# Kernel tuning notes

Measured on AMD Instinct MI355X. Metric: run time of the kernel, lower is better.

Reference implementation:

```python
import jax, jax.numpy as jnp
import numpy as np
from jax import lax

B, C_IN, C_OUT, K, N_W, L = 32, 256, 256, 7, 8, 4096
SQ = C_IN // 32  # squeezed dim = 8
STRIDE, PAD = 1, 3


def setup_inputs() -> dict:
    key = jax.random.key(0)
    ks = jax.random.split(key, 8)
    s = 0.05
    return {
        "x": jax.random.normal(ks[0], (B, C_IN, L), dtype=jnp.float32),
        "conv_weight": jax.random.normal(ks[1], (C_OUT, C_IN, K, N_W), dtype=jnp.float32) * s,
        "w1": jax.random.normal(ks[2], (C_IN, SQ), dtype=jnp.float32) * s,   # linear1 weight (x @ w1)
        "b1": jax.random.normal(ks[3], (SQ,), dtype=jnp.float32) * s,
        "wk": jax.random.normal(ks[4], (SQ, K), dtype=jnp.float32) * s,      # kernel head
        "wi": jax.random.normal(ks[5], (SQ, C_IN), dtype=jnp.float32) * s,   # inc head
        "wo": jax.random.normal(ks[6], (SQ, C_OUT), dtype=jnp.float32) * s,  # outc head
        "wn": jax.random.normal(ks[7], (SQ, N_W), dtype=jnp.float32) * s,    # nums head
    }


def reference(x, conv_weight, w1, b1, wk, wi, wo, wn):
    # SqueezeFeedForward: AdaptiveAvgPool1d(1) == mean over length, then Linear + exact GELU
    pooled = jnp.mean(x, axis=-1)                        # [B, C_in]
    h = jax.nn.gelu(pooled @ w1 + b1, approximate=False)  # [B, SQ]

    kr = jax.nn.sigmoid(h @ wk)          # [B, K]
    inc = jax.nn.sigmoid(h @ wi)         # [B, C_in]
    outc = jax.nn.sigmoid(h @ wo)        # [B, C_out]
    nums = jax.nn.softmax(h @ wn, -1)    # [B, N_w]

    # Per-sample mixed weights: sum over num_weight of 4-way outer-product gated base weight
    w = jnp.einsum('bk,bi,bo,bn,oikn->boik', kr, inc, outc, nums, conv_weight)  # [B,O,I,K]

    b, o, i, k = w.shape
    l = x.shape[-1]
    # Batched per-sample conv via grouped conv: groups = B
    lhs = x.reshape(1, b * i, l)         # [1, B*I, L]
    rhs = w.reshape(b * o, i, k)         # [B*O, I, K]
    out = lax.conv_general_dilated(
        lhs, rhs,
        window_strides=(STRIDE,),
        padding=[(PAD, PAD)],
        dimension_numbers=('NCH', 'OIH', 'NCH'),
        feature_group_count=b,
    )
    return out.reshape(b, o, -1)         # [B, O, L_out]
```

## Files before the change

### kernel.cpp

```cpp
#include <hip/hip_runtime.h>
#include <hip/hip_bf16.h>
#include <math.h>

#define B_   32
#define CI   256
#define CO   256
#define KW   7
#define NW   8
#define SQD  8
#define L_   4096
#define PITCH 272

typedef __attribute__((ext_vector_type(8))) __bf16 bf16x8;
typedef __attribute__((ext_vector_type(4))) __bf16 bf16x4;
typedef __attribute__((ext_vector_type(4))) float  f32x4;

static __device__ __forceinline__ unsigned short f2bf(float f) {
    unsigned int u = __builtin_bit_cast(unsigned int, f);
    u += 0x7FFFu + ((u >> 16) & 1u);
    return (unsigned short)(u >> 16);
}
static __device__ __forceinline__ uint2 pack4bf(float a, float b, float c, float d) {
    bf16x4 v;
    v[0] = (__bf16)a; v[1] = (__bf16)b; v[2] = (__bf16)c; v[3] = (__bf16)d;
    return __builtin_bit_cast(uint2, v);
}

__global__ __launch_bounds__(256) void k1_mean(
        const float* __restrict__ x, float* __restrict__ pooled) {
    int row = blockIdx.x;
    const float* p = x + (size_t)row * L_;
    int t = threadIdx.x;
    float s = 0.f;
#pragma unroll
    for (int it = 0; it < 4; ++it) {
        float4 v = *(const float4*)(p + (size_t)(t + 256 * it) * 4);
        s += v.x + v.y + v.z + v.w;
    }
    for (int m = 1; m <= 32; m <<= 1) s += __shfl_xor(s, m);
    __shared__ float wsum[4];
    if ((t & 63) == 0) wsum[t >> 6] = s;
    __syncthreads();
    if (t == 0)
        pooled[row] = (wsum[0] + wsum[1] + wsum[2] + wsum[3]) * (1.0f / L_);
}

__global__ __launch_bounds__(64) void k2_gates(
        const float* __restrict__ pooled,
        const float* __restrict__ w1, const float* __restrict__ b1,
        const float* __restrict__ wk, const float* __restrict__ wi,
        const float* __restrict__ wo, const float* __restrict__ wn,
        float* __restrict__ kr, float* __restrict__ inc,
        float* __restrict__ outc, float* __restrict__ nums)
{
    int b = blockIdx.x, lane = threadIdx.x;
    float pc[4];
#pragma unroll
    for (int j = 0; j < 4; ++j)
        pc[j] = pooled[b * CI + lane + 64 * j];
    float h[SQD];
#pragma unroll
    for (int s = 0; s < SQD; ++s) {
        float ps = 0.f;
#pragma unroll
        for (int j = 0; j < 4; ++j)
            ps += pc[j] * w1[(lane + 64 * j) * SQD + s];
        for (int m = 1; m <= 32; m <<= 1) ps += __shfl_xor(ps, m);
        float z = ps + b1[s];
        h[s] = 0.5f * z * (1.0f + erff(z * 0.70710678118654752f));
    }
    if (lane < KW) {
        float a = 0.f;
#pragma unroll
        for (int s = 0; s < SQD; ++s) a += h[s] * wk[s * KW + lane];
        kr[b * 8 + lane] = 1.0f / (1.0f + expf(-a));
    }
    if (lane < NW) {
        float e[NW]; float mx = -1e30f;
#pragma unroll
        for (int n = 0; n < NW; ++n) {
            float a = 0.f;
#pragma unroll
            for (int s = 0; s < SQD; ++s) a += h[s] * wn[s * NW + n];
            e[n] = a; mx = fmaxf(mx, a);
        }
        float den = 0.f;
#pragma unroll
        for (int n = 0; n < NW; ++n) den += expf(e[n] - mx);
        nums[b * NW + lane] = expf(e[lane] - mx) / den;
    }
#pragma unroll
    for (int j = 0; j < 4; ++j) {
        int c = lane + 64 * j;
        float a = 0.f, o2 = 0.f;
#pragma unroll
        for (int s = 0; s < SQD; ++s) {
            a  += h[s] * wi[s * CI + c];
            o2 += h[s] * wo[s * CO + c];
        }
        inc[b * CI + c]  = 1.0f / (1.0f + expf(-a));
        outc[b * CO + c] = 1.0f / (1.0f + expf(-o2));
    }
}

__global__ __launch_bounds__(256) void k3_wgen(
        const float* __restrict__ cw,
        const float* __restrict__ kr, const float* __restrict__ inc,
        const float* __restrict__ outc, const float* __restrict__ nums,
        unsigned short* __restrict__ W2) {
    __shared__ float s_nums[B_][NW];
    __shared__ float s_kr[B_][KW];
    __shared__ float s_inc[B_][32];
    __shared__ float s_outc[B_][8];
    int t = threadIdx.x;
    int ic = blockIdx.x & 7, o0 = (blockIdx.x >> 3) * 8;
    s_nums[t >> 3][t & 7] = nums[t];
    if (t < B_ * KW) s_kr[t / KW][t % KW] = kr[(t / KW) * 8 + (t % KW)];
    for (int u = t; u < 32 * 32; u += 256) {
        int bb = u >> 5, ii = u & 31;
        s_inc[bb][ii] = inc[bb * CI + ic * 32 + ii];
    }
    for (int u = t; u < 32 * 8; u += 256) {
        int bb = u >> 3, oo = u & 7;
        s_outc[bb][oo] = outc[bb * CO + o0 + oo];
    }
    __syncthreads();
    int ii = t & 31, oo = t >> 5;
    int o = o0 + oo, i = ic * 32 + ii;
    float cwv[KW][NW];
    const float* p = cw + ((size_t)(o * CI + i)) * (KW * NW);
#pragma unroll
    for (int k = 0; k < KW; ++k)
#pragma unroll
        for (int n = 0; n < NW; ++n) cwv[k][n] = p[k * NW + n];
    for (int bb = 0; bb < B_; ++bb) {
        float gio = s_inc[bb][ii] * s_outc[bb][oo];
#pragma unroll
        for (int k = 0; k < KW; ++k) {
            float sk = 0.f;
#pragma unroll
            for (int n = 0; n < NW; ++n) sk += s_nums[bb][n] * cwv[k][n];
            float w = s_kr[bb][k] * gio * sk;
            W2[(((size_t)(bb * KW + k) * 8 + ic) * CO + o) * 32 + ii] = f2bf(w);
        }
    }
}

__global__ __launch_bounds__(256, 2) void k4_conv(
        const float* __restrict__ x,
        const unsigned short* __restrict__ W2,
        float* __restrict__ out) {
    __shared__ __align__(16) unsigned short xs[134 * PITCH];
    int bid = blockIdx.x;
    int wg  = (bid & 7) * 128 + (bid >> 3);
    int b = wg >> 5, l0 = (wg & 31) * 128;
    int t = threadIdx.x;
    const float* xb = x + (size_t)b * CI * L_;

    {
        int u = t >> 3;
        int lam = t & 7;
        int i0 = u * 8;
#pragma unroll
        for (int it = 0; it < 4; ++it) {
            int ch = lam + 8 * it;
            const float* src = xb + (size_t)i0 * L_ + l0 + ch * 4;
            float4 f[8];
#pragma unroll
            for (int e = 0; e < 8; ++e)
                f[e] = *(const float4*)(src + (size_t)e * L_);
#pragma unroll
            for (int j = 0; j < 4; ++j) {
                int r = ch * 4 + j + 3;
                uint2 a = pack4bf((&f[0].x)[j], (&f[1].x)[j], (&f[2].x)[j], (&f[3].x)[j]);
                uint2 c = pack4bf((&f[4].x)[j], (&f[5].x)[j], (&f[6].x)[j], (&f[7].x)[j]);
                uint4 w; w.x = a.x; w.y = a.y; w.z = c.x; w.w = c.y;
                *(uint4*)(xs + r * PITCH + u * 8) = w;
            }
        }
    }
    if (t < 192) {
        int h = t >> 5, u = t & 31;
        int r = (h < 3) ? h : (128 + h);
        int gl = l0 - 3 + r;
        bool ok = (gl >= 0 && gl < L_);
        float f[8];
#pragma unroll
        for (int e = 0; e < 8; ++e)
            f[e] = ok ? xb[(size_t)(u * 8 + e) * L_ + gl] : 0.f;
        uint2 a = pack4bf(f[0], f[1], f[2], f[3]);
        uint2 c = pack4bf(f[4], f[5], f[6], f[7]);
        uint4 w; w.x = a.x; w.y = a.y; w.z = c.x; w.w = c.y;
        *(uint4*)(xs + r * PITCH + u * 8) = w;
    }
    __syncthreads();

    int lane = t & 63, wid = t >> 6;
    int o_half = (wid & 1) * 128;
    int l_half = (wid >> 1) * 64;
    int ml = lane & 15, kg = lane >> 4;

    f32x4 acc[8][4];
#pragma unroll
    for (int a = 0; a < 8; ++a)
#pragma unroll
        for (int c = 0; c < 4; ++c) acc[a][c] = (f32x4){0.f, 0.f, 0.f, 0.f};

    const unsigned short* wA = W2 + (size_t)b * (56 * CO * 32)
                               + (o_half + ml) * 32 + kg * 8;
    const unsigned short* xB = xs + (size_t)(l_half + ml) * PITCH + kg * 8;

    auto LOADF = [&](bf16x8 (&AF)[8], bf16x8 (&BF)[4], int S) {
        int k_ = S >> 3, icc_ = S & 7;
#pragma unroll
        for (int mt = 0; mt < 8; ++mt)
            AF[mt] = *(const bf16x8*)(wA + (size_t)S * (CO * 32) + mt * 16 * 32);
#pragma unroll
        for (int nt = 0; nt < 4; ++nt)
            BF[nt] = *(const bf16x8*)(xB + (nt * 16 + k_) * PITCH + icc_ * 32);
    };
    auto DOMFMA = [&](bf16x8 (&AF)[8], bf16x8 (&BF)[4]) {
        __builtin_amdgcn_s_setprio(1);
#pragma unroll
        for (int mt = 0; mt < 8; ++mt)
#pragma unroll
            for (int nt = 0; nt < 4; ++nt)
                acc[mt][nt] = __builtin_amdgcn_mfma_f32_16x16x32_bf16(
                    AF[mt], BF[nt], acc[mt][nt], 0, 0, 0);
        __builtin_amdgcn_s_setprio(0);
    };

    bf16x8 afA[8], bfA[4], afB[8], bfB[4];
    LOADF(afA, bfA, 0);
    for (int s = 0; s < 56; s += 2) {
        LOADF(afB, bfB, s + 1);
        DOMFMA(afA, bfA);
        if (s + 2 < 56) LOADF(afA, bfA, s + 2);
        DOMFMA(afB, bfB);
    }

#pragma unroll
    for (int mt = 0; mt < 8; ++mt) {
        int o = o_half + mt * 16 + kg * 4;
#pragma unroll
        for (int nt = 0; nt < 4; ++nt) {
            int l = l0 + l_half + nt * 16 + ml;
            float* po = out + ((size_t)(b * CO + o)) * L_ + l;
#pragma unroll
            for (int q = 0; q < 4; ++q)
                po[(size_t)q * L_] = acc[mt][nt][q];
        }
    }
}

extern "C" void kernel_launch(void* const* d_in, const int* in_sizes, int n_in,
                              void* d_out, int out_size, void* d_ws, size_t ws_size,
                              hipStream_t stream) {
    const float* x  = (const float*)d_in[0];
    const float* cw = (const float*)d_in[1];
    const float* w1 = (const float*)d_in[2];
    const float* b1 = (const float*)d_in[3];
    const float* wk = (const float*)d_in[4];
    const float* wi = (const float*)d_in[5];
    const float* wo = (const float*)d_in[6];
    const float* wn = (const float*)d_in[7];
    float* out = (float*)d_out;

    char* ws = (char*)d_ws;
    unsigned short* W2 = (unsigned short*)(ws + 0);
    float* pooled = (float*)(ws + 29360128);
    float* kr     = (float*)(ws + 29392896);
    float* inc    = (float*)(ws + 29393920);
    float* outc   = (float*)(ws + 29426688);
    float* nums   = (float*)(ws + 29459456);

    k1_mean<<<B_ * CI, 256, 0, stream>>>(x, pooled);
    k2_gates<<<B_, 64, 0, stream>>>(pooled, w1, b1, wk, wi, wo, wn,
                                    kr, inc, outc, nums);
    k3_wgen<<<256, 256, 0, stream>>>(cw, kr, inc, outc, nums, W2);
    k4_conv<<<1024, 256, 0, stream>>>(x, W2, out);
}
```

Baseline: 189.4 us.

## Switch conv GEMM to 32x32x16 MFMA with per-wave 64-channel output tiles

Replaces the 16x16x32 bf16 MFMA tiling, where each wave owned a 128x64 output block, with 32x32x16 MFMA and each wave owning 64 output channels across all 128 positions. The K loop is split into 112 half-steps, and each wave starts at a different offset (wid*28) so waves read different weight and LDS regions at the same time. The aim is fewer fragment loads per MFMA, better operand reuse and less LDS bank contention. In exchange the output stores follow the 32x32 accumulator layout, which may coalesce less well, and the wrap-around indexing adds a little scalar work.

```diff
diff --git a/kernel.cpp b/kernel.cpp
--- a/kernel.cpp
+++ b/kernel.cpp
@@ -11,9 +11,10 @@
 #define L_   4096
 #define PITCH 272
 
-typedef __attribute__((ext_vector_type(8))) __bf16 bf16x8;
-typedef __attribute__((ext_vector_type(4))) __bf16 bf16x4;
-typedef __attribute__((ext_vector_type(4))) float  f32x4;
+typedef __attribute__((ext_vector_type(8)))  __bf16 bf16x8;
+typedef __attribute__((ext_vector_type(4)))  __bf16 bf16x4;
+typedef __attribute__((ext_vector_type(4)))  float  f32x4;
+typedef __attribute__((ext_vector_type(16))) float  f32x16;
 
 static __device__ __forceinline__ unsigned short f2bf(float f) {
     unsigned int u = __builtin_bit_cast(unsigned int, f);
@@ -196,61 +197,68 @@
     __syncthreads();
 
     int lane = t & 63, wid = t >> 6;
-    int o_half = (wid & 1) * 128;
-    int l_half = (wid >> 1) * 64;
-    int ml = lane & 15, kg = lane >> 4;
-
-    f32x4 acc[8][4];
-#pragma unroll
-    for (int a = 0; a < 8; ++a)
-#pragma unroll
-        for (int c = 0; c < 4; ++c) acc[a][c] = (f32x4){0.f, 0.f, 0.f, 0.f};
+    int o_base = wid * 64;
+    int ml = lane & 31, khalf = lane >> 5;
+
+    f32x16 acc[2][4];
+#pragma unroll
+    for (int a = 0; a < 2; ++a)
+#pragma unroll
+        for (int c = 0; c < 4; ++c)
+#pragma unroll
+            for (int q = 0; q < 16; ++q) acc[a][c][q] = 0.f;
 
     const unsigned short* wA = W2 + (size_t)b * (56 * CO * 32)
-                               + (o_half + ml) * 32 + kg * 8;
-    const unsigned short* xB = xs + (size_t)(l_half + ml) * PITCH + kg * 8;
-
-    auto LOADF = [&](bf16x8 (&AF)[8], bf16x8 (&BF)[4], int S) {
-        int k_ = S >> 3, icc_ = S & 7;
-#pragma unroll
-        for (int mt = 0; mt < 8; ++mt)
-            AF[mt] = *(const bf16x8*)(wA + (size_t)S * (CO * 32) + mt * 16 * 32);
+                               + (o_base + ml) * 32 + khalf * 8;
+    const unsigned short* xB = xs + (size_t)ml * PITCH + khalf * 8;
+
+    auto LOADF = [&](bf16x8 (&AF)[2], bf16x8 (&BF)[4], int S) {
+        int k_ = S >> 4, icc_ = (S >> 1) & 7, half_ = S & 1;
+        size_t aoff = (size_t)(k_ * 8 + icc_) * (CO * 32) + half_ * 16;
+#pragma unroll
+        for (int mt = 0; mt < 2; ++mt)
+            AF[mt] = *(const bf16x8*)(wA + aoff + mt * 32 * 32);
+        int boff = k_ * PITCH + icc_ * 32 + half_ * 16;
 #pragma unroll
         for (int nt = 0; nt < 4; ++nt)
-            BF[nt] = *(const bf16x8*)(xB + (nt * 16 + k_) * PITCH + icc_ * 32);
+            BF[nt] = *(const bf16x8*)(xB + boff + nt * 32 * PITCH);
     };
-    auto DOMFMA = [&](bf16x8 (&AF)[8], bf16x8 (&BF)[4]) {
+    auto DOMFMA = [&](bf16x8 (&AF)[2], bf16x8 (&BF)[4]) {
         __builtin_amdgcn_s_setprio(1);
 #pragma unroll
-        for (int mt = 0; mt < 8; ++mt)
+        for (int mt = 0; mt < 2; ++mt)
 #pragma unroll
             for (int nt = 0; nt < 4; ++nt)
-                acc[mt][nt] = __builtin_amdgcn_mfma_f32_16x16x32_bf16(
+                acc[mt][nt] = __builtin_amdgcn_mfma_f32_32x32x16_bf16(
                     AF[mt], BF[nt], acc[mt][nt], 0, 0, 0);
         __builtin_amdgcn_s_setprio(0);
     };
 
-    bf16x8 afA[8], bfA[4], afB[8], bfB[4];
-    LOADF(afA, bfA, 0);
-    for (int s = 0; s < 56; s += 2) {
-        LOADF(afB, bfB, s + 1);
+    int base = wid * 28;
+    bf16x8 afA[2], bfA[4], afB[2], bfB[4];
+    LOADF(afA, bfA, base);
+    for (int ss = 0; ss < 112; ss += 2) {
+        int S1 = ss + 1 + base; if (S1 >= 112) S1 -= 112;
+        LOADF(afB, bfB, S1);
         DOMFMA(afA, bfA);
-        if (s + 2 < 56) LOADF(afA, bfA, s + 2);
+        if (ss + 2 < 112) {
+            int S2 = ss + 2 + base; if (S2 >= 112) S2 -= 112;
+            LOADF(afA, bfA, S2);
+        }
         DOMFMA(afB, bfB);
     }
 
 #pragma unroll
-    for (int mt = 0; mt < 8; ++mt) {
-        int o = o_half + mt * 16 + kg * 4;
+    for (int mt = 0; mt < 2; ++mt)
 #pragma unroll
         for (int nt = 0; nt < 4; ++nt) {
-            int l = l0 + l_half + nt * 16 + ml;
-            float* po = out + ((size_t)(b * CO + o)) * L_ + l;
-#pragma unroll
-            for (int q = 0; q < 4; ++q)
-                po[(size_t)q * L_] = acc[mt][nt][q];
-        }
-    }
+            int l = l0 + nt * 32 + ml;
+#pragma unroll
+            for (int q = 0; q < 16; ++q) {
+                int o = o_base + mt * 32 + (q & 3) + 8 * (q >> 2) + 4 * khalf;
+                out[((size_t)(b * CO + o)) * L_ + l] = acc[mt][nt][q];
+            }
+        }
 }
 
 extern "C" void kernel_launch(void* const* d_in, const int* in_sizes, int n_in,
```

After: 194.5 us. 1.03x slower.

## Switch conv GEMM to 32x32x16 MFMA with per-wave full-O tiles

Applied to the files above, without the earlier changes.

Replaces the 16x16x32 bf16 MFMA tiling, where each wave covered a 128(O)x64(L) quadrant, with 32x32x16 MFMAs where each wave covers all 256 output channels for a 32-wide L strip. This reduces B-fragment LDS reads per MFMA and changes the weight-fragment and output-store addressing to match the 32x32 accumulator layout. The LDS pitch also changes from 272 to 264, which may alter bank conflicts. Every wave now reads the full weight slab from global/L2, doubling weight traffic per wave, and the K-loop has twice as many steps.

```diff
diff --git a/kernel.cpp b/kernel.cpp
--- a/kernel.cpp
+++ b/kernel.cpp
@@ -9,11 +9,11 @@
 #define NW   8
 #define SQD  8
 #define L_   4096
-#define PITCH 272
-
-typedef __attribute__((ext_vector_type(8))) __bf16 bf16x8;
-typedef __attribute__((ext_vector_type(4))) __bf16 bf16x4;
-typedef __attribute__((ext_vector_type(4))) float  f32x4;
+#define PITCH 264
+
+typedef __attribute__((ext_vector_type(8)))  __bf16 bf16x8;
+typedef __attribute__((ext_vector_type(4)))  __bf16 bf16x4;
+typedef __attribute__((ext_vector_type(16))) float  f32x16;
 
 static __device__ __forceinline__ unsigned short f2bf(float f) {
     unsigned int u = __builtin_bit_cast(unsigned int, f);
@@ -196,59 +196,54 @@
     __syncthreads();
 
     int lane = t & 63, wid = t >> 6;
-    int o_half = (wid & 1) * 128;
-    int l_half = (wid >> 1) * 64;
-    int ml = lane & 15, kg = lane >> 4;
-
-    f32x4 acc[8][4];
+    int l_wave = wid * 32;
+    int ml = lane & 31, khalf = lane >> 5;
+
+    f32x16 acc[8];
 #pragma unroll
     for (int a = 0; a < 8; ++a)
 #pragma unroll
-        for (int c = 0; c < 4; ++c) acc[a][c] = (f32x4){0.f, 0.f, 0.f, 0.f};
+        for (int q = 0; q < 16; ++q) acc[a][q] = 0.f;
 
     const unsigned short* wA = W2 + (size_t)b * (56 * CO * 32)
-                               + (o_half + ml) * 32 + kg * 8;
-    const unsigned short* xB = xs + (size_t)(l_half + ml) * PITCH + kg * 8;
-
-    auto LOADF = [&](bf16x8 (&AF)[8], bf16x8 (&BF)[4], int S) {
-        int k_ = S >> 3, icc_ = S & 7;
+                               + ml * 32 + khalf * 8;
+    const unsigned short* xB = xs + (size_t)(l_wave + ml) * PITCH + khalf * 8;
+
+    auto LOADF = [&](bf16x8 (&AF)[8], bf16x8& BF, int S) {
+        int k_ = S >> 4, icc_ = (S >> 1) & 7, half_ = S & 1;
+        const unsigned short* ap = wA + (size_t)(k_ * 8 + icc_) * (CO * 32)
+                                   + half_ * 16;
 #pragma unroll
         for (int mt = 0; mt < 8; ++mt)
-            AF[mt] = *(const bf16x8*)(wA + (size_t)S * (CO * 32) + mt * 16 * 32);
-#pragma unroll
-        for (int nt = 0; nt < 4; ++nt)
-            BF[nt] = *(const bf16x8*)(xB + (nt * 16 + k_) * PITCH + icc_ * 32);
+            AF[mt] = *(const bf16x8*)(ap + mt * 32 * 32);
+        BF = *(const bf16x8*)(xB + k_ * PITCH + icc_ * 32 + half_ * 16);
     };
-    auto DOMFMA = [&](bf16x8 (&AF)[8], bf16x8 (&BF)[4]) {
+    auto DOMFMA = [&](bf16x8 (&AF)[8], bf16x8& BF) {
         __builtin_amdgcn_s_setprio(1);
 #pragma unroll
         for (int mt = 0; mt < 8; ++mt)
-#pragma unroll
-            for (int nt = 0; nt < 4; ++nt)
-                acc[mt][nt] = __builtin_amdgcn_mfma_f32_16x16x32_bf16(
-                    AF[mt], BF[nt], acc[mt][nt], 0, 0, 0);
+            acc[mt] = __builtin_amdgcn_mfma_f32_32x32x16_bf16(
+                AF[mt], BF, acc[mt], 0, 0, 0);
         __builtin_amdgcn_s_setprio(0);
     };
 
-    bf16x8 afA[8], bfA[4], afB[8], bfB[4];
+    bf16x8 afA[8], afB[8];
+    bf16x8 bfA, bfB;
     LOADF(afA, bfA, 0);
-    for (int s = 0; s < 56; s += 2) {
-        LOADF(afB, bfB, s + 1);
+    for (int S = 0; S < 112; S += 2) {
+        LOADF(afB, bfB, S + 1);
         DOMFMA(afA, bfA);
-        if (s + 2 < 56) LOADF(afA, bfA, s + 2);
+        if (S + 2 < 112) LOADF(afA, bfA, S + 2);
         DOMFMA(afB, bfB);
     }
 
 #pragma unroll
     for (int mt = 0; mt < 8; ++mt) {
-        int o = o_half + mt * 16 + kg * 4;
-#pragma unroll
-        for (int nt = 0; nt < 4; ++nt) {
-            int l = l0 + l_half + nt * 16 + ml;
-            float* po = out + ((size_t)(b * CO + o)) * L_ + l;
-#pragma unroll
-            for (int q = 0; q < 4; ++q)
-                po[(size_t)q * L_] = acc[mt][nt][q];
+        int l = l0 + l_wave + ml;
+#pragma unroll
+        for (int q = 0; q < 16; ++q) {
+            int o = mt * 32 + (q & 3) + 8 * (q >> 2) + 4 * khalf;
+            out[((size_t)(b * CO + o)) * L_ + l] = acc[mt][q];
         }
     }
 }
```

Measured after the change: 282.7 us. +49.2%, slower.
